# Kernel optimization log

Measured on AMD Instinct MI355X. Metric: run time of the kernel, lower is better.

## Reference

```python
import jax, jax.numpy as jnp
import numpy as np
from jax import lax

B, T, E, H = 32, 512, 256, 512

def setup_inputs() -> dict:
    key = jax.random.key(0)
    ks = jax.random.split(key, 7)
    s = 1.0 / np.sqrt(H)  # PyTorch RNN init range
    u = lambda k, sh: jax.random.uniform(k, sh, jnp.float32, -s, s)
    return {
        "xs": jax.random.normal(ks[0], (B, T, E), jnp.float32),
        "w_ih0": u(ks[1], (2, H, E)),      # [dir, H, in]
        "w_hh0": u(ks[2], (2, H, H)),
        "b0":    u(ks[3], (2, 2, H)),      # [dir, (b_ih,b_hh), H]
        "w_ih1": u(ks[4], (2, H, 2 * H)),
        "w_hh1": u(ks[5], (2, H, H)),
        "b1":    u(ks[6], (2, 2, H)),
    }

def _rnn_dir(x_tbi, w_ih, w_hh, b_ih, b_hh, reverse):
    # Precompute the input GEMM for all timesteps: [T,B,H]
    pre = jnp.einsum('tbi,hi->tbh', x_tbi, w_ih) + b_ih + b_hh
    h0 = jnp.zeros((x_tbi.shape[1], w_hh.shape[0]), x_tbi.dtype)
    def step(h, p):
        h = jnp.tanh(p + h @ w_hh.T)
        return h, h
    _, hs = lax.scan(step, h0, pre, reverse=reverse)  # ys aligned with xs order
    hy = hs[0] if reverse else hs[-1]
    return hs, hy

def _layer(x_tbi, w_ih, w_hh, b):
    hf, hyf = _rnn_dir(x_tbi, w_ih[0], w_hh[0], b[0, 0], b[0, 1], False)
    hb, hyb = _rnn_dir(x_tbi, w_ih[1], w_hh[1], b[1, 0], b[1, 1], True)
    return jnp.concatenate([hf, hb], axis=-1), jnp.stack([hyf, hyb])

def reference(xs, w_ih0, w_hh0, b0, w_ih1, w_hh1, b1):
    x = jnp.transpose(xs, (1, 0, 2))          # batch_first -> [T,B,E]
    h1, hy0 = _layer(x, w_ih0, w_hh0, b0)     # [T,B,2H], [2,B,H]
    h2, hy1 = _layer(h1, w_ih1, w_hh1, b1)
    hs = jnp.transpose(h2, (1, 0, 2))         # [B,T,2H]
    hy = jnp.concatenate([hy0, hy1], axis=0)  # [4,B,H] layer-major like PyTorch
    # F.dropout with p=0.0 is identity
    return (hs, hy)
```

## Files before the change

kernel.cpp:

```cpp
#include <hip/hip_runtime.h>
#include <hip/hip_fp16.h>


#define T_ 512
#define B_ 32
#define E_ 256
#define H_ 512

using half8 = _Float16 __attribute__((ext_vector_type(8)));
using f32x4 = float __attribute__((ext_vector_type(4)));
typedef unsigned long long u64;
typedef unsigned int u32;

static constexpr size_t OFF_PRE   = 0;
static constexpr size_t OFF_XH1   = 32ull << 20;
static constexpr size_t OFF_X0H   = 64ull << 20;
static constexpr size_t OFF_W0H   = 72ull << 20;
static constexpr size_t OFF_W1H   = OFF_W0H + (512ull << 10);
static constexpr size_t OFF_WHH   = OFF_W1H + (2ull << 20);
static constexpr size_t OFF_BS    = OFF_WHH + (2ull << 20);
static constexpr size_t OFF_HX    = OFF_BS + (8ull << 10);
static constexpr size_t ZERO_SIZE = 512ull << 10;

__device__ __forceinline__ float fast_tanh(float x) {
    float cx = fminf(fmaxf(x, -9.0f), 9.0f);
    float e2 = __expf(2.0f * cx);
    return (e2 - 1.0f) * __builtin_amdgcn_rcpf(e2 + 1.0f);
}

__global__ void prep_kernel(const float* __restrict__ xs,
                            const float* __restrict__ wih0,
                            const float* __restrict__ whh0,
                            const float* __restrict__ b0,
                            const float* __restrict__ wih1,
                            const float* __restrict__ whh1,
                            const float* __restrict__ b1,
                            _Float16* __restrict__ x0h,
                            _Float16* __restrict__ w0h,
                            _Float16* __restrict__ w1h,
                            _Float16* __restrict__ whh,
                            float* __restrict__ bsum)
{
    const int N0 = T_ * B_ * E_;
    const int N1 = 2 * H_ * E_;
    const int N2 = 2 * H_ * 2*H_;
    const int N3 = 2 * H_ * H_;
    const int total = N0 + N1 + N2 + 2 * N3 + 2048;
    for (int idx = blockIdx.x * blockDim.x + threadIdx.x; idx < total;
         idx += gridDim.x * blockDim.x) {
        int i = idx;
        if (i < N0) {
            int t = i >> 13;
            int r = i & 8191;
            int b = r >> 8;
            int e = r & 255;
            x0h[i] = (_Float16)xs[((size_t)(b << 9) + t) * 256 + e];
        } else if ((i -= N0) < N1) {
            w0h[i] = (_Float16)wih0[i];
        } else if ((i -= N1) < N2) {
            w1h[i] = (_Float16)wih1[i];
        } else if ((i -= N2) < N3) {
            whh[i] = (_Float16)whh0[i];
        } else if ((i -= N3) < N3) {
            whh[N3 + i] = (_Float16)whh1[i];
        } else {
            i -= N3;
            int layer = i >> 10;
            int r = i & 1023;
            int d = r >> 9;
            int j = r & 511;
            const float* bb = layer ? b1 : b0;
            bsum[i] = bb[d * 1024 + j] + bb[d * 1024 + 512 + j];
        }
    }
}

__global__ __launch_bounds__(256, 2)
void gemm_kernel(const _Float16* __restrict__ X,
                 const _Float16* __restrict__ W,
                 const float* __restrict__ bias,
                 _Float16* __restrict__ out, int K)
{
    __shared__ _Float16 Ash[64][72];
    __shared__ _Float16 Bsh[64][72];
    const int m0 = blockIdx.x * 64, n0 = blockIdx.y * 64, d = blockIdx.z;
    const _Float16* Wd = W + (size_t)d * 512 * K;
    const int tid = threadIdx.x;
    const int l = tid & 63, w = tid >> 6;
    const int wm = w & 1, wn = w >> 1;
    const int lm = l & 15, q = l >> 4;
    f32x4 c[2][2] = {};
    for (int kk = 0; kk < K; kk += 64) {
        for (int ci = tid; ci < 512; ci += 256) {
            int row = ci >> 3, col = (ci & 7) * 8;
            *(half8*)&Ash[row][col] =
                *(const half8*)&X[(size_t)(m0 + row) * K + kk + col];
            *(half8*)&Bsh[row][col] =
                *(const half8*)&Wd[(size_t)(n0 + row) * K + kk + col];
        }
        __syncthreads();
        for (int kt = 0; kt < 2; ++kt) {
            const int kof = kt * 32 + q * 8;
            half8 a0 = *(const half8*)&Ash[wm * 32 + lm][kof];
            half8 a1 = *(const half8*)&Ash[wm * 32 + 16 + lm][kof];
            half8 b0f = *(const half8*)&Bsh[wn * 32 + lm][kof];
            half8 b1f = *(const half8*)&Bsh[wn * 32 + 16 + lm][kof];
            c[0][0] = __builtin_amdgcn_mfma_f32_16x16x32_f16(a0, b0f, c[0][0], 0, 0, 0);
            c[0][1] = __builtin_amdgcn_mfma_f32_16x16x32_f16(a0, b1f, c[0][1], 0, 0, 0);
            c[1][0] = __builtin_amdgcn_mfma_f32_16x16x32_f16(a1, b0f, c[1][0], 0, 0, 0);
            c[1][1] = __builtin_amdgcn_mfma_f32_16x16x32_f16(a1, b1f, c[1][1], 0, 0, 0);
        }
        __syncthreads();
    }
    _Float16* outd = out + (size_t)d * 16384 * 512;
    for (int mi = 0; mi < 2; ++mi)
        for (int ni = 0; ni < 2; ++ni) {
            int col = n0 + wn * 32 + ni * 16 + lm;
            float bv = bias[d * 512 + col];
            for (int r = 0; r < 4; ++r) {
                int rowm = m0 + wm * 32 + mi * 16 + q * 4 + r;
                outd[(size_t)rowm * 512 + col] = (_Float16)(c[mi][ni][r] + bv);
            }
        }
}

__global__ __launch_bounds__(256)
void rnn_kernel(const _Float16* __restrict__ pre,
                const _Float16* __restrict__ whh,
                u64* __restrict__ hx,
                _Float16* __restrict__ xh1,
                float* __restrict__ dout,
                int layer)
{
    __shared__ uint4 As[64 * 33];
    const int gid = blockIdx.x;
    const int d = gid >> 4, g = gid & 15;
    const int tid = threadIdx.x, wv = tid >> 6, l = tid & 63;
    const int lm = l & 15, q = l >> 4;
    const int wm = wv & 1, wn = wv >> 1;
    const int jn = g * 32 + wn * 16;
    const int bA = wm * 16 + lm;
    const int bq = wm * 16 + q * 4;

    half8 Bf[16];
    {
        const _Float16* wrow = whh + ((size_t)d * 512 + jn + lm) * 512;
#pragma unroll
        for (int kt = 0; kt < 16; ++kt)
            Bf[kt] = *(const half8*)&wrow[kt * 32 + q * 8];
    }

    u64* hbd = hx + (size_t)d * 2 * 8192;
    const int jp_pub = (jn + (lm & ~1)) >> 1;
    const int scat_base = ((tid >> 2) * 33) * 4 + (tid & 3);
    u32* AsW = (u32*)As;

    for (int s = 0; s < T_; ++s) {
        const int t = d ? (T_ - 1 - s) : s;

        const _Float16* prow = pre + ((size_t)d * 16384 + (size_t)t * B_) * 512 + jn + lm;
        _Float16 pv[4];
#pragma unroll
        for (int r = 0; r < 4; ++r)
            pv[r] = prow[(size_t)(bq + r) * 512];

        const u64* src = hbd + (size_t)(s & 1) * 8192 + tid;
        const unsigned tag = (unsigned)s;
        u64 wvv[32];
        bool stale = true;
        do {
#pragma unroll
            for (int i = 0; i < 32; ++i)
                wvv[i] = __hip_atomic_load(&src[i * 256],
                                           __ATOMIC_RELAXED, __HIP_MEMORY_SCOPE_SYSTEM);
            bool ok = true;
#pragma unroll
            for (int i = 0; i < 32; ++i)
                ok &= ((unsigned)(wvv[i] >> 32) == tag);
            stale = __any(!ok);
        } while (stale);

        __syncthreads();
#pragma unroll
        for (int i = 0; i < 32; ++i)
            AsW[scat_base + i * 4] = (u32)wvv[i];
        __syncthreads();

        f32x4 c0, c1;
#pragma unroll
        for (int r = 0; r < 4; ++r) { c0[r] = (float)pv[r]; c1[r] = 0.0f; }
#pragma unroll
        for (int kt = 0; kt < 16; ++kt) {
            union { uint4 u; half8 h; } cv;
            cv.u = As[(kt * 4 + q) * 33 + bA];
            if (kt & 1) c1 = __builtin_amdgcn_mfma_f32_16x16x32_f16(cv.h, Bf[kt], c1, 0, 0, 0);
            else        c0 = __builtin_amdgcn_mfma_f32_16x16x32_f16(cv.h, Bf[kt], c0, 0, 0, 0);
        }

        u64* dst = hbd + (size_t)((s + 1) & 1) * 8192;
        const u64 tagw = ((u64)(unsigned)(s + 1)) << 32;
        const int j = jn + lm;
        float hv[4];
        unsigned hb[4];
#pragma unroll
        for (int r = 0; r < 4; ++r) {
            hv[r] = fast_tanh(c0[r] + c1[r]);
            union { _Float16 f; unsigned short u; } cb;
            cb.f = (_Float16)hv[r];
            hb[r] = cb.u;
        }
#pragma unroll
        for (int r = 0; r < 4; ++r) {
            unsigned p = __shfl_xor(hb[r], 1, 64);
            unsigned lo = (l & 1) ? p : hb[r];
            unsigned hi = (l & 1) ? hb[r] : p;
            if ((r >> 1) == (l & 1)) {
                u64 word = tagw | ((u64)hi << 16) | lo;
                __hip_atomic_store(&dst[(size_t)(bq + r) * 256 + jp_pub], word,
                                   __ATOMIC_RELAXED, __HIP_MEMORY_SCOPE_SYSTEM);
            }
        }
#pragma unroll
        for (int r = 0; r < 4; ++r) {
            const int b = bq + r;
            if (layer == 0) {
                xh1[((size_t)t * B_ + b) * 1024 + d * 512 + j] = (_Float16)hv[r];
            } else {
                dout[((size_t)b * T_ + t) * 1024 + d * 512 + j] = hv[r];
            }
            if (s == T_ - 1) {
                dout[16777216ull + ((size_t)(layer * 2 + d) * B_ + b) * 512 + j] = hv[r];
            }
        }
    }
}

extern "C" void kernel_launch(void* const* d_in, const int* in_sizes, int n_in,
                              void* d_out, int out_size, void* d_ws, size_t ws_size,
                              hipStream_t stream)
{
    const float* xs   = (const float*)d_in[0];
    const float* wih0 = (const float*)d_in[1];
    const float* whh0 = (const float*)d_in[2];
    const float* b0   = (const float*)d_in[3];
    const float* wih1 = (const float*)d_in[4];
    const float* whh1 = (const float*)d_in[5];
    const float* b1   = (const float*)d_in[6];

    char* ws = (char*)d_ws;
    _Float16* pre  = (_Float16*)(ws + OFF_PRE);
    _Float16* xh1  = (_Float16*)(ws + OFF_XH1);
    _Float16* x0h  = (_Float16*)(ws + OFF_X0H);
    _Float16* w0h  = (_Float16*)(ws + OFF_W0H);
    _Float16* w1h  = (_Float16*)(ws + OFF_W1H);
    _Float16* whh  = (_Float16*)(ws + OFF_WHH);
    float*    bsum = (float*)(ws + OFF_BS);
    u64*      hx   = (u64*)(ws + OFF_HX);
    float*    out  = (float*)d_out;

    (void)hipMemsetAsync(ws + OFF_HX, 0, ZERO_SIZE, stream);

    prep_kernel<<<2048, 256, 0, stream>>>(xs, wih0, whh0, b0, wih1, whh1, b1,
                                          x0h, w0h, w1h, whh, bsum);

    gemm_kernel<<<dim3(256, 8, 2), 256, 0, stream>>>(x0h, w0h, bsum, pre, 256);
    rnn_kernel<<<32, 256, 0, stream>>>(pre, whh, hx, xh1, out, 0);

    gemm_kernel<<<dim3(256, 8, 2), 256, 0, stream>>>(xh1, w1h, bsum + 1024, pre, 1024);
    rnn_kernel<<<32, 256, 0, stream>>>(pre, whh + 2 * 512 * 512,
                                       hx + 2 * 2 * 8192, xh1, out, 2  == 2 ? 1 : 1);
}
```

Measured before the change: 2.901 ms.

## Pin each RNN direction to a single XCD and sync via per-block step flags

The recurrent kernel now launches 256 blocks. Each block reads its hardware XCC id and takes a slot on that die. The first two dies that fill 16 slots are given the forward and backward directions, and every other block exits, so all blocks exchanging hidden state for one direction share an L2. Each block publishes a per-step flag that the others poll before reading the tagged hidden-state words. Memory scope drops from system to agent, and LDS is double-buffered so one barrier per step can be removed. This relies on the hardware scheduling 16 blocks per XCD and on agent-scope coherence across blocks. A 10M-iteration fallback makes waiting blocks exit, which could leave a direction underpopulated and deadlock.

```diff
diff --git a/kernel.cpp b/kernel.cpp
--- a/kernel.cpp
+++ b/kernel.cpp
@@ -20,7 +20,12 @@
 static constexpr size_t OFF_WHH   = OFF_W1H + (2ull << 20);
 static constexpr size_t OFF_BS    = OFF_WHH + (2ull << 20);
 static constexpr size_t OFF_HX    = OFF_BS + (8ull << 10);
-static constexpr size_t ZERO_SIZE = 512ull << 10;
+static constexpr size_t OFF_FLG   = OFF_HX + (512ull << 10);
+static constexpr size_t OFF_CTL   = OFF_FLG + 512;
+static constexpr size_t ZERO_SIZE = (512ull << 10) + 1024;
+
+static constexpr size_t HX_LAYER_STRIDE = 2 * 2 * 32 * 256;
+static constexpr size_t HX_DIR_STRIDE   = 2 * 32 * 256;
 
 __device__ __forceinline__ float fast_tanh(float x) {
     float cx = fminf(fmaxf(x, -9.0f), 9.0f);
@@ -128,14 +133,51 @@
 void rnn_kernel(const _Float16* __restrict__ pre,
                 const _Float16* __restrict__ whh,
                 u64* __restrict__ hx,
+                u32* __restrict__ flgL,
+                u32* __restrict__ ctl,
                 _Float16* __restrict__ xh1,
                 float* __restrict__ dout,
                 int layer)
 {
-    __shared__ uint4 As[64 * 33];
-    const int gid = blockIdx.x;
-    const int d = gid >> 4, g = gid & 15;
-    const int tid = threadIdx.x, wv = tid >> 6, l = tid & 63;
+    __shared__ uint4 As[2][64 * 33];
+    __shared__ int sh_role, sh_slot;
+
+    const int tid = threadIdx.x;
+
+    if (tid == 0) {
+        int xcc;
+        asm volatile("s_getreg_b32 %0, hwreg(HW_REG_XCC_ID)" : "=s"(xcc));
+        xcc &= 7;
+        u32 slot = __hip_atomic_fetch_add(&ctl[xcc], 1u, __ATOMIC_RELAXED,
+                                          __HIP_MEMORY_SCOPE_SYSTEM);
+        int role = 0;
+        if (slot < 16u) {
+            if (slot == 15u) {
+                u32 r = __hip_atomic_fetch_add(&ctl[8], 1u, __ATOMIC_ACQ_REL,
+                                               __HIP_MEMORY_SCOPE_SYSTEM);
+                role = (r < 2u) ? (int)r + 1 : 3;
+                __hip_atomic_store(&ctl[16 + xcc], (u32)role, __ATOMIC_RELEASE,
+                                   __HIP_MEMORY_SCOPE_SYSTEM);
+            } else {
+                long it = 0;
+                while (true) {
+                    u32 r = __hip_atomic_load(&ctl[16 + xcc], __ATOMIC_ACQUIRE,
+                                              __HIP_MEMORY_SCOPE_SYSTEM);
+                    if (r) { role = (int)r; break; }
+                    if (++it > 10000000) { role = 3; break; }
+                }
+            }
+        }
+        sh_role = role;
+        sh_slot = (int)slot;
+    }
+    __syncthreads();
+    const int role = sh_role;
+    const int g = sh_slot;
+    if (role == 0 || role == 3) return;
+    const int d = role - 1;
+
+    const int wv = tid >> 6, l = tid & 63;
     const int lm = l & 15, q = l >> 4;
     const int wm = wv & 1, wn = wv >> 1;
     const int jn = g * 32 + wn * 16;
@@ -150,10 +192,10 @@
             Bf[kt] = *(const half8*)&wrow[kt * 32 + q * 8];
     }
 
-    u64* hbd = hx + (size_t)d * 2 * 8192;
+    u64* hbd = hx + (size_t)d * HX_DIR_STRIDE;
+    u32* flg = flgL + d * 32;
     const int jp_pub = (jn + (lm & ~1)) >> 1;
     const int scat_base = ((tid >> 2) * 33) * 4 + (tid & 3);
-    u32* AsW = (u32*)As;
 
     for (int s = 0; s < T_; ++s) {
         const int t = d ? (T_ - 1 - s) : s;
@@ -163,6 +205,18 @@
 #pragma unroll
         for (int r = 0; r < 4; ++r)
             pv[r] = prow[(size_t)(bq + r) * 512];
+
+        {
+            const u32 need = (u32)s;
+            bool ok;
+            do {
+                u32 f = (l < 16)
+                    ? __hip_atomic_load(&flg[l], __ATOMIC_RELAXED,
+                                        __HIP_MEMORY_SCOPE_AGENT)
+                    : 0xFFFFFFFFu;
+                ok = __all(f >= need);
+            } while (!ok);
+        }
 
         const u64* src = hbd + (size_t)(s & 1) * 8192 + tid;
         const unsigned tag = (unsigned)s;
@@ -172,7 +226,7 @@
 #pragma unroll
             for (int i = 0; i < 32; ++i)
                 wvv[i] = __hip_atomic_load(&src[i * 256],
-                                           __ATOMIC_RELAXED, __HIP_MEMORY_SCOPE_SYSTEM);
+                                           __ATOMIC_RELAXED, __HIP_MEMORY_SCOPE_AGENT);
             bool ok = true;
 #pragma unroll
             for (int i = 0; i < 32; ++i)
@@ -180,7 +234,7 @@
             stale = __any(!ok);
         } while (stale);
 
-        __syncthreads();
+        u32* AsW = (u32*)&As[s & 1][0];
 #pragma unroll
         for (int i = 0; i < 32; ++i)
             AsW[scat_base + i * 4] = (u32)wvv[i];
@@ -192,7 +246,7 @@
 #pragma unroll
         for (int kt = 0; kt < 16; ++kt) {
             union { uint4 u; half8 h; } cv;
-            cv.u = As[(kt * 4 + q) * 33 + bA];
+            cv.u = As[s & 1][(kt * 4 + q) * 33 + bA];
             if (kt & 1) c1 = __builtin_amdgcn_mfma_f32_16x16x32_f16(cv.h, Bf[kt], c1, 0, 0, 0);
             else        c0 = __builtin_amdgcn_mfma_f32_16x16x32_f16(cv.h, Bf[kt], c0, 0, 0, 0);
         }
@@ -217,9 +271,14 @@
             if ((r >> 1) == (l & 1)) {
                 u64 word = tagw | ((u64)hi << 16) | lo;
                 __hip_atomic_store(&dst[(size_t)(bq + r) * 256 + jp_pub], word,
-                                   __ATOMIC_RELAXED, __HIP_MEMORY_SCOPE_SYSTEM);
-            }
-        }
+                                   __ATOMIC_RELAXED, __HIP_MEMORY_SCOPE_AGENT);
+            }
+        }
+        __syncthreads();
+        if (tid == 0)
+            __hip_atomic_store(&flg[g], (u32)(s + 1), __ATOMIC_RELAXED,
+                               __HIP_MEMORY_SCOPE_AGENT);
+
 #pragma unroll
         for (int r = 0; r < 4; ++r) {
             const int b = bq + r;
@@ -256,6 +315,8 @@
     _Float16* whh  = (_Float16*)(ws + OFF_WHH);
     float*    bsum = (float*)(ws + OFF_BS);
     u64*      hx   = (u64*)(ws + OFF_HX);
+    u32*      flg  = (u32*)(ws + OFF_FLG);
+    u32*      ctl  = (u32*)(ws + OFF_CTL);
     float*    out  = (float*)d_out;
 
     (void)hipMemsetAsync(ws + OFF_HX, 0, ZERO_SIZE, stream);
@@ -264,9 +325,10 @@
                                           x0h, w0h, w1h, whh, bsum);
 
     gemm_kernel<<<dim3(256, 8, 2), 256, 0, stream>>>(x0h, w0h, bsum, pre, 256);
-    rnn_kernel<<<32, 256, 0, stream>>>(pre, whh, hx, xh1, out, 0);
+    rnn_kernel<<<256, 256, 0, stream>>>(pre, whh, hx, flg, ctl, xh1, out, 0);
 
     gemm_kernel<<<dim3(256, 8, 2), 256, 0, stream>>>(xh1, w1h, bsum + 1024, pre, 1024);
-    rnn_kernel<<<32, 256, 0, stream>>>(pre, whh + 2 * 512 * 512,
-                                       hx + 2 * 2 * 8192, xh1, out, 2  == 2 ? 1 : 1);
-}
+    rnn_kernel<<<256, 256, 0, stream>>>(pre, whh + 2 * 512 * 512,
+                                        hx + HX_LAYER_STRIDE, flg + 64, ctl + 32,
+                                        xh1, out, 1);
+}
```

After: 3.133 ms. 1.08x slower.
